# Kernel tuning notes

Hardware: AMD Instinct MI355X
Metric: run time of the kernel (lower is better)

The kernel has to match this reference:

```python
import jax, jax.numpy as jnp
import numpy as np

N = 50000        # nodes
E = 800000       # edges
H = 128          # in = hidden = out width
L = 4            # num_layers
BN_EPS = 1e-5


def _bn(x, g, b):
    # training-mode batch norm over the node dimension (biased variance, as torch)
    mu = jnp.mean(x, axis=0)
    var = jnp.mean((x - mu) ** 2, axis=0)
    return (x - mu) * jax.lax.rsqrt(var + BN_EPS) * g + b


def setup_inputs() -> dict:
    key = jax.random.key(0)
    ks = jax.random.split(key, 16)
    s = 0.05
    return {
        "x": jax.random.normal(ks[0], (N, H), dtype=jnp.float32),
        "edge_index": jax.random.randint(ks[1], (2, E), 0, N, dtype=jnp.int32),
        # stacked per-layer MLP params (all layers share dims H->H->H)
        "fc1_w": jax.random.normal(ks[2], (L, H, H), dtype=jnp.float32) * s,
        "fc1_b": jnp.zeros((L, H), dtype=jnp.float32),
        "bn1_g": jnp.ones((L, H), dtype=jnp.float32),
        "bn1_b": jnp.zeros((L, H), dtype=jnp.float32),
        "fc2_w": jax.random.normal(ks[3], (L, H, H), dtype=jnp.float32) * s,
        "fc2_b": jnp.zeros((L, H), dtype=jnp.float32),
        "bn2_g": jnp.ones((L, H), dtype=jnp.float32),
        "bn2_b": jnp.zeros((L, H), dtype=jnp.float32),
        # outer per-layer BatchNorm (intended one-per-GIN-layer)
        "bn3_g": jnp.ones((L, H), dtype=jnp.float32),
        "bn3_b": jnp.zeros((L, H), dtype=jnp.float32),
        # final classifier
        "fc_w": jax.random.normal(ks[4], (H, H), dtype=jnp.float32) * s,
        "fc_b": jnp.zeros((H,), dtype=jnp.float32),
    }


def reference(x, edge_index, fc1_w, fc1_b, bn1_g, bn1_b, fc2_w, fc2_b,
              bn2_g, bn2_b, bn3_g, bn3_b, fc_w, fc_b):
    src = edge_index[0]
    dst = edge_index[1]
    for i in range(L):
        # GINConv, eps=0: h = MLP((1+eps)*x + sum_{j in N(v)} x_j)
        agg = jax.ops.segment_sum(x[src], dst, num_segments=N)  # [N, H]
        h = x + agg
        # MLP: relu(bn1(fc1(h))) -> bn2(fc2(.))
        h = jax.nn.relu(_bn(h @ fc1_w[i].T + fc1_b[i], bn1_g[i], bn1_b[i]))
        h = _bn(h @ fc2_w[i].T + fc2_b[i], bn2_g[i], bn2_b[i])
        # outer BN + ReLU per layer
        x = jax.nn.relu(_bn(h, bn3_g[i], bn3_b[i]))
    return x @ fc_w.T + fc_b  # [N, H]
```

## Files before the change

kernel.cpp:

```cpp
#include <hip/hip_runtime.h>
#include <hip/hip_bf16.h>

#define NN 50000
#define HD 128
#define NL 4
#define BN_EPS 1e-5f
#define NTILES 3125

typedef __attribute__((ext_vector_type(8))) short short8;
typedef __attribute__((ext_vector_type(4))) float f32x4;

__device__ inline ushort f2bf(float f){
  uint u = __float_as_uint(f);
  uint r = (u + 0x7fffu + ((u >> 16) & 1u)) >> 16;
  return (ushort)r;
}
__device__ inline float bflo(uint u){ return __uint_as_float(u << 16); }
__device__ inline float bfhi(uint u){ return __uint_as_float(u & 0xffff0000u); }

__global__ void cast_f32_bf16x4(const float* __restrict__ in, ushort* __restrict__ out, int n4){
  int i = blockIdx.x * blockDim.x + threadIdx.x;
  int stride = gridDim.x * blockDim.x;
  const float4* in4 = (const float4*)in;
  for (; i < n4; i += stride){
    float4 v = in4[i];
    ushort4 r;
    r.x = f2bf(v.x); r.y = f2bf(v.y); r.z = f2bf(v.z); r.w = f2bf(v.w);
    *(ushort4*)(out + i * 4) = r;
  }
}

__global__ void cast_weights(const float* __restrict__ w1, const float* __restrict__ w2,
                             const float* __restrict__ wf, ushort* __restrict__ wb){
  int i = blockIdx.x * 256 + threadIdx.x;
  if (i >= 36864) return;
  const float* src;
  if (i < 16384)      src = w1 + i * 4;
  else if (i < 32768) src = w2 + (i - 16384) * 4;
  else                src = wf + (i - 32768) * 4;
  float4 v = *(const float4*)src;
  ushort4 r;
  r.x = f2bf(v.x); r.y = f2bf(v.y); r.z = f2bf(v.z); r.w = f2bf(v.w);
  *(ushort4*)(wb + i * 4) = r;
}

__global__ void fill1_kernel(const int* __restrict__ dst, int* __restrict__ cnt,
                             int* __restrict__ pos, int E){
  int e = (blockIdx.x * 256 + threadIdx.x) * 4;
  if (e + 4 <= E){
    int4 d = *(const int4*)(dst + e);
    int4 p;
    p.x = atomicAdd(&cnt[d.x], 1);
    p.y = atomicAdd(&cnt[d.y], 1);
    p.z = atomicAdd(&cnt[d.z], 1);
    p.w = atomicAdd(&cnt[d.w], 1);
    *(int4*)(pos + e) = p;
  } else {
    for (; e < E; ++e) pos[e] = atomicAdd(&cnt[dst[e]], 1);
  }
}

__global__ void scan1_kernel(const int* __restrict__ deg, int* __restrict__ incl,
                             int* __restrict__ bsum, int n){
  __shared__ int tmp[1024];
  int gid = blockIdx.x * 1024 + threadIdx.x;
  int v = (gid < n) ? deg[gid] : 0;
  tmp[threadIdx.x] = v;
  __syncthreads();
  for (int ofs = 1; ofs < 1024; ofs <<= 1){
    int t = tmp[threadIdx.x];
    int a = (threadIdx.x >= ofs) ? tmp[threadIdx.x - ofs] : 0;
    __syncthreads();
    tmp[threadIdx.x] = t + a;
    __syncthreads();
  }
  if (gid < n) incl[gid] = tmp[threadIdx.x];
  if (threadIdx.x == 1023) bsum[blockIdx.x] = tmp[1023];
}

__global__ void scan2_kernel(const int* __restrict__ bsum, int* __restrict__ base,
                             int* __restrict__ off, int nb, int n){
  if (threadIdx.x == 0){
    int run = 0;
    for (int i = 0; i < nb; ++i){ base[i] = run; run += bsum[i]; }
    off[n] = run;
  }
}

__global__ void scan3_kernel(const int* __restrict__ deg, const int* __restrict__ incl,
                             const int* __restrict__ base, int* __restrict__ off, int n){
  int gid = blockIdx.x * 1024 + threadIdx.x;
  if (gid < n) off[gid] = incl[gid] - deg[gid] + base[blockIdx.x];
}

__global__ void fill2_kernel(const int* __restrict__ src, const int* __restrict__ dst,
                             const int* __restrict__ off, const int* __restrict__ pos,
                             int* __restrict__ csrc, int E){
  int e = (blockIdx.x * 256 + threadIdx.x) * 4;
  if (e + 4 <= E){
    int4 d = *(const int4*)(dst + e);
    int4 p = *(const int4*)(pos + e);
    int4 s = *(const int4*)(src + e);
    csrc[off[d.x] + p.x] = s.x;
    csrc[off[d.y] + p.y] = s.y;
    csrc[off[d.z] + p.z] = s.z;
    csrc[off[d.w] + p.w] = s.w;
  } else {
    for (; e < E; ++e) csrc[off[dst[e]] + pos[e]] = src[e];
  }
}

__device__ inline void bn_params_tid(const float* st, const float* gA, const float* gB,
                                     const float* bB, int mode, float* sS, float* sT){
  int c = threadIdx.x;
  if (c < 128){
    const float invN = 1.f / (float)NN;
    float mu = st[c] * invN;
    float var = fmaxf(st[128 + c] * invN - mu * mu, 0.f);
    float S, T;
    if (mode == 0){
      S = gA[c] * rsqrtf(var + BN_EPS);
      T = gB[c] - mu * S;
    } else {
      float inv2 = rsqrtf(var + BN_EPS);
      float tt = gA[c] * inv2;
      float inv3 = rsqrtf(tt * tt * var + BN_EPS);
      S = tt * inv3 * gB[c];
      T = bB[c] - mu * S;
    }
    sS[c] = S; sT[c] = T;
  }
}

__global__ __launch_bounds__(256) void agg_kernel(const ushort* __restrict__ xb,
                                                  const int* __restrict__ off,
                                                  const int* __restrict__ csrc,
                                                  ushort* __restrict__ h){
  int node = blockIdx.x * 4 + (threadIdx.x >> 6);
  int lane = threadIdx.x & 63;
  const uint* xr = (const uint*)xb;
  uint self = xr[node * 64 + lane];
  float ax = bflo(self), ay = bfhi(self);
  int s = off[node], e = off[node + 1];
  int j = s;
  for (; j + 8 <= e; j += 8){
    uint v0 = xr[csrc[j+0]*64+lane], v1 = xr[csrc[j+1]*64+lane];
    uint v2 = xr[csrc[j+2]*64+lane], v3 = xr[csrc[j+3]*64+lane];
    uint v4 = xr[csrc[j+4]*64+lane], v5 = xr[csrc[j+5]*64+lane];
    uint v6 = xr[csrc[j+6]*64+lane], v7 = xr[csrc[j+7]*64+lane];
    ax += bflo(v0)+bflo(v1)+bflo(v2)+bflo(v3)+bflo(v4)+bflo(v5)+bflo(v6)+bflo(v7);
    ay += bfhi(v0)+bfhi(v1)+bfhi(v2)+bfhi(v3)+bfhi(v4)+bfhi(v5)+bfhi(v6)+bfhi(v7);
  }
  for (; j + 4 <= e; j += 4){
    uint v0 = xr[csrc[j+0]*64+lane], v1 = xr[csrc[j+1]*64+lane];
    uint v2 = xr[csrc[j+2]*64+lane], v3 = xr[csrc[j+3]*64+lane];
    ax += bflo(v0)+bflo(v1)+bflo(v2)+bflo(v3);
    ay += bfhi(v0)+bfhi(v1)+bfhi(v2)+bfhi(v3);
  }
  for (; j < e; ++j){
    uint v = xr[csrc[j] * 64 + lane];
    ax += bflo(v); ay += bfhi(v);
  }
  uint o = (uint)f2bf(ax) | ((uint)f2bf(ay) << 16);
  ((uint*)h)[node * 64 + lane] = o;
}

__global__ __launch_bounds__(256) void agg_bn_kernel(const ushort* __restrict__ yb,
                                                     const int* __restrict__ off,
                                                     const int* __restrict__ csrc,
                                                     const float* __restrict__ statsIn,
                                                     const float* __restrict__ g2,
                                                     const float* __restrict__ g3,
                                                     const float* __restrict__ b3,
                                                     ushort* __restrict__ h){
  __shared__ float sS[128];
  __shared__ float sT[128];
  bn_params_tid(statsIn, g2, g3, b3, 1, sS, sT);
  __syncthreads();
  int node = blockIdx.x * 4 + (threadIdx.x >> 6);
  int lane = threadIdx.x & 63;
  float S0 = sS[lane*2], T0 = sT[lane*2];
  float S1 = sS[lane*2+1], T1 = sT[lane*2+1];
  const uint* xr = (const uint*)yb;
  uint self = xr[node * 64 + lane];
  float ax = fmaxf(bflo(self)*S0+T0, 0.f), ay = fmaxf(bfhi(self)*S1+T1, 0.f);
  int s = off[node], e = off[node + 1];
  int j = s;
  for (; j + 4 <= e; j += 4){
    uint v0 = xr[csrc[j+0]*64+lane], v1 = xr[csrc[j+1]*64+lane];
    uint v2 = xr[csrc[j+2]*64+lane], v3 = xr[csrc[j+3]*64+lane];
    ax += fmaxf(bflo(v0)*S0+T0,0.f) + fmaxf(bflo(v1)*S0+T0,0.f)
        + fmaxf(bflo(v2)*S0+T0,0.f) + fmaxf(bflo(v3)*S0+T0,0.f);
    ay += fmaxf(bfhi(v0)*S1+T1,0.f) + fmaxf(bfhi(v1)*S1+T1,0.f)
        + fmaxf(bfhi(v2)*S1+T1,0.f) + fmaxf(bfhi(v3)*S1+T1,0.f);
  }
  for (; j < e; ++j){
    uint v = xr[csrc[j] * 64 + lane];
    ax += fmaxf(bflo(v)*S0+T0,0.f);
    ay += fmaxf(bfhi(v)*S1+T1,0.f);
  }
  uint o = (uint)f2bf(ax) | ((uint)f2bf(ay) << 16);
  ((uint*)h)[node * 64 + lane] = o;
}

__global__ __launch_bounds__(512) void gemm_kernel(const ushort* __restrict__ A,
                                                   const ushort* __restrict__ W,
                                                   const float* __restrict__ bias,
                                                   ushort* __restrict__ Yb,
                                                   float* __restrict__ Yf,
                                                   float* __restrict__ statsOut,
                                                   const float* __restrict__ statsIn,
                                                   const float* __restrict__ gA,
                                                   const float* __restrict__ gB,
                                                   const float* __restrict__ bB,
                                                   int mode){
  __shared__ uint4 w4[128 * 17];
  __shared__ float ssum[128];
  __shared__ float ssq[128];
  __shared__ float sS[128];
  __shared__ float sT[128];
  const uint4* Wg = (const uint4*)W;
  for (int c = threadIdx.x; c < 2048; c += 512){
    w4[(c >> 4) * 17 + (c & 15)] = Wg[c];
  }
  if (statsIn) bn_params_tid(statsIn, gA, gB, bB, mode, sS, sT);
  if (threadIdx.x < 128){ ssum[threadIdx.x] = 0.f; ssq[threadIdx.x] = 0.f; }
  __syncthreads();

  int wave = threadIdx.x >> 6;
  int lane = threadIdx.x & 63;
  int m = lane & 15, q = lane >> 4;
  int tile = blockIdx.x * 8 + wave;
  bool tv = tile < NTILES;
  const uint4* A4 = (const uint4*)A;

  f32x4 acc[8];
#pragma unroll
  for (int i = 0; i < 8; ++i) acc[i] = (f32x4)0.f;

#pragma unroll
  for (int kt = 0; kt < 4; ++kt){
    short8 af = (short8)0;
    if (tv){
      uint4 t = A4[(tile * 16 + m) * 16 + kt * 4 + q];
      if (statsIn){
        int kc = kt * 32 + q * 8;
        uint4 pk;
        pk.x = (uint)f2bf(fmaxf(bflo(t.x)*sS[kc+0]+sT[kc+0],0.f))
             | ((uint)f2bf(fmaxf(bfhi(t.x)*sS[kc+1]+sT[kc+1],0.f)) << 16);
        pk.y = (uint)f2bf(fmaxf(bflo(t.y)*sS[kc+2]+sT[kc+2],0.f))
             | ((uint)f2bf(fmaxf(bfhi(t.y)*sS[kc+3]+sT[kc+3],0.f)) << 16);
        pk.z = (uint)f2bf(fmaxf(bflo(t.z)*sS[kc+4]+sT[kc+4],0.f))
             | ((uint)f2bf(fmaxf(bfhi(t.z)*sS[kc+5]+sT[kc+5],0.f)) << 16);
        pk.w = (uint)f2bf(fmaxf(bflo(t.w)*sS[kc+6]+sT[kc+6],0.f))
             | ((uint)f2bf(fmaxf(bfhi(t.w)*sS[kc+7]+sT[kc+7],0.f)) << 16);
        t = pk;
      }
      af = *(short8*)&t;
    }
#pragma unroll
    for (int to = 0; to < 8; ++to){
      uint4 bw = w4[(to * 16 + m) * 17 + kt * 4 + q];
      acc[to] = __builtin_amdgcn_mfma_f32_16x16x32_bf16(af, *(short8*)&bw, acc[to], 0, 0, 0);
    }
  }

  bool dost = (statsOut != nullptr);
#pragma unroll
  for (int to = 0; to < 8; ++to){
    int col = to * 16 + m;
    float bc = bias[col];
    float ls = 0.f, lq = 0.f;
    if (tv){
#pragma unroll
      for (int r = 0; r < 4; ++r){
        float v = acc[to][r] + bc;
        int row = tile * 16 + q * 4 + r;
        if (Yb) Yb[row * 128 + col] = __builtin_bit_cast(ushort, f2bf(v));
        else    Yf[row * 128 + col] = v;
        ls += v; lq += v * v;
      }
    }
    if (dost){
      ls += __shfl_xor(ls, 16); lq += __shfl_xor(lq, 16);
      ls += __shfl_xor(ls, 32); lq += __shfl_xor(lq, 32);
      if (tv && q == 0){ atomicAdd(&ssum[col], ls); atomicAdd(&ssq[col], lq); }
    }
  }
  if (dost){
    __syncthreads();
    if (threadIdx.x < 128){
      atomicAdd(&statsOut[threadIdx.x], ssum[threadIdx.x]);
      atomicAdd(&statsOut[128 + threadIdx.x], ssq[threadIdx.x]);
    }
  }
}

extern "C" void kernel_launch(void* const* d_in, const int* in_sizes, int n_in,
                              void* d_out, int out_size, void* d_ws, size_t ws_size,
                              hipStream_t stream) {
  const float* x     = (const float*)d_in[0];
  const int*   ei    = (const int*)d_in[1];
  const float* fc1_w = (const float*)d_in[2];
  const float* fc1_b = (const float*)d_in[3];
  const float* bn1_g = (const float*)d_in[4];
  const float* bn1_b = (const float*)d_in[5];
  const float* fc2_w = (const float*)d_in[6];
  const float* fc2_b = (const float*)d_in[7];
  const float* bn2_g = (const float*)d_in[8];
  const float* bn3_g = (const float*)d_in[10];
  const float* bn3_b = (const float*)d_in[11];
  const float* fc_w  = (const float*)d_in[12];
  const float* fc_b  = (const float*)d_in[13];

  int E = in_sizes[1] / 2;
  const int* srcp = ei;
  const int* dstp = ei + E;

  char* ws = (char*)d_ws;
  int*    off    = (int*)(ws + 0);
  int*    cnt    = (int*)(ws + 200064);
  int*    pos    = (int*)(ws + 400128);
  int*    csrc   = (int*)(ws + 3600128);
  ushort* wb     = (ushort*)(ws + 6800128);
  float*  stats  = (float*)(ws + 7095040);
  int*    sscr   = (int*)(ws + 7103232);
  ushort* xb     = (ushort*)(ws + 7104256);
  ushort* hb     = (ushort*)(ws + 19904256);
  ushort* y1b    = (ushort*)(ws + 32704256);
  ushort* y2b    = (ushort*)(ws + 45504256);

  int* incl = csrc;
  int* bsum = sscr;
  int* base = sscr + 64;

  hipMemsetAsync(cnt, 0, 200064, stream);
  hipMemsetAsync(stats, 0, 8192, stream);

  cast_f32_bf16x4<<<2048, 256, 0, stream>>>(x, xb, NN * HD / 4);
  cast_weights<<<144, 256, 0, stream>>>(fc1_w, fc2_w, fc_w, wb);

  const int EB4 = (E / 4 + 255) / 256 + 1;
  const int SB = (NN + 1023) / 1024;
  fill1_kernel<<<EB4, 256, 0, stream>>>(dstp, cnt, pos, E);
  scan1_kernel<<<SB, 1024, 0, stream>>>(cnt, incl, bsum, NN);
  scan2_kernel<<<1, 64, 0, stream>>>(bsum, base, off, SB, NN);
  scan3_kernel<<<SB, 1024, 0, stream>>>(cnt, incl, base, off, NN);
  fill2_kernel<<<EB4, 256, 0, stream>>>(srcp, dstp, off, pos, csrc, E);

  const int gb = (NTILES + 7) / 8;

  for (int i = 0; i < NL; ++i){
    if (i == 0){
      agg_kernel<<<NN / 4, 256, 0, stream>>>(xb, off, csrc, hb);
    } else {
      agg_bn_kernel<<<NN / 4, 256, 0, stream>>>(y2b, off, csrc,
                                                stats + (i - 1) * 512 + 256,
                                                bn2_g + (i - 1) * 128,
                                                bn3_g + (i - 1) * 128,
                                                bn3_b + (i - 1) * 128, hb);
    }
    gemm_kernel<<<gb, 512, 0, stream>>>(hb, wb + i * 16384, fc1_b + i * 128,
                                        y1b, nullptr, stats + i * 512,
                                        nullptr, nullptr, nullptr, nullptr, 0);
    gemm_kernel<<<gb, 512, 0, stream>>>(y1b, wb + 65536 + i * 16384, fc2_b + i * 128,
                                        y2b, nullptr, stats + i * 512 + 256,
                                        stats + i * 512, bn1_g + i * 128,
                                        bn1_b + i * 128, nullptr, 0);
  }

  gemm_kernel<<<gb, 512, 0, stream>>>(y2b, wb + 131072, fc_b,
                                      nullptr, (float*)d_out, nullptr,
                                      stats + 3 * 512 + 256, bn2_g + 384,
                                      bn3_g + 384, bn3_b + 384, 1);
}
```

Before: 486.3 us.

## Derive BN1 stats from Gram matrix and fuse both MLP GEMMs per layer

BN1 mean and variance are now computed algebraically from the Gram matrix H^T H and the column sums of the aggregated features, plus the fc1 weights. This lets fc1, BN1, ReLU, fc2 and the BN2 stat accumulation run in one fused kernel with no y1 round trip through global memory. The CSR degree counters are also striped four ways per node to cut atomic contention in graph construction. The cost is extra Gram, reduce and param kernels per layer, and bias handling that assumes the fc1 bias cancels under batch norm.

```diff
diff --git a/kernel.cpp b/kernel.cpp
--- a/kernel.cpp
+++ b/kernel.cpp
@@ -6,6 +6,9 @@
 #define NL 4
 #define BN_EPS 1e-5f
 #define NTILES 3125
+#define N4 200000
+#define GBLK 256
+#define GROWS 196
 
 typedef __attribute__((ext_vector_type(8))) short short8;
 typedef __attribute__((ext_vector_type(4))) float f32x4;
@@ -44,19 +47,19 @@
   *(ushort4*)(wb + i * 4) = r;
 }
 
-__global__ void fill1_kernel(const int* __restrict__ dst, int* __restrict__ cnt,
+__global__ void fill1_kernel(const int* __restrict__ dst, int* __restrict__ cnt4,
                              int* __restrict__ pos, int E){
   int e = (blockIdx.x * 256 + threadIdx.x) * 4;
   if (e + 4 <= E){
     int4 d = *(const int4*)(dst + e);
     int4 p;
-    p.x = atomicAdd(&cnt[d.x], 1);
-    p.y = atomicAdd(&cnt[d.y], 1);
-    p.z = atomicAdd(&cnt[d.z], 1);
-    p.w = atomicAdd(&cnt[d.w], 1);
+    p.x = atomicAdd(&cnt4[d.x * 4 + 0], 1);
+    p.y = atomicAdd(&cnt4[d.y * 4 + 1], 1);
+    p.z = atomicAdd(&cnt4[d.z * 4 + 2], 1);
+    p.w = atomicAdd(&cnt4[d.w * 4 + 3], 1);
     *(int4*)(pos + e) = p;
   } else {
-    for (; e < E; ++e) pos[e] = atomicAdd(&cnt[dst[e]], 1);
+    for (; e < E; ++e) pos[e] = atomicAdd(&cnt4[dst[e] * 4 + (e & 3)], 1);
   }
 }
 
@@ -94,19 +97,19 @@
 }
 
 __global__ void fill2_kernel(const int* __restrict__ src, const int* __restrict__ dst,
-                             const int* __restrict__ off, const int* __restrict__ pos,
+                             const int* __restrict__ off4, const int* __restrict__ pos,
                              int* __restrict__ csrc, int E){
   int e = (blockIdx.x * 256 + threadIdx.x) * 4;
   if (e + 4 <= E){
     int4 d = *(const int4*)(dst + e);
     int4 p = *(const int4*)(pos + e);
     int4 s = *(const int4*)(src + e);
-    csrc[off[d.x] + p.x] = s.x;
-    csrc[off[d.y] + p.y] = s.y;
-    csrc[off[d.z] + p.z] = s.z;
-    csrc[off[d.w] + p.w] = s.w;
+    csrc[off4[d.x * 4 + 0] + p.x] = s.x;
+    csrc[off4[d.y * 4 + 1] + p.y] = s.y;
+    csrc[off4[d.z * 4 + 2] + p.z] = s.z;
+    csrc[off4[d.w * 4 + 3] + p.w] = s.w;
   } else {
-    for (; e < E; ++e) csrc[off[dst[e]] + pos[e]] = src[e];
+    for (; e < E; ++e) csrc[off4[dst[e] * 4 + (e & 3)] + pos[e]] = src[e];
   }
 }
 
@@ -133,7 +136,7 @@
 }
 
 __global__ __launch_bounds__(256) void agg_kernel(const ushort* __restrict__ xb,
-                                                  const int* __restrict__ off,
+                                                  const int* __restrict__ off4,
                                                   const int* __restrict__ csrc,
                                                   ushort* __restrict__ h){
   int node = blockIdx.x * 4 + (threadIdx.x >> 6);
@@ -141,7 +144,7 @@
   const uint* xr = (const uint*)xb;
   uint self = xr[node * 64 + lane];
   float ax = bflo(self), ay = bfhi(self);
-  int s = off[node], e = off[node + 1];
+  int s = off4[node * 4], e = off4[node * 4 + 4];
   int j = s;
   for (; j + 8 <= e; j += 8){
     uint v0 = xr[csrc[j+0]*64+lane], v1 = xr[csrc[j+1]*64+lane];
@@ -166,7 +169,7 @@
 }
 
 __global__ __launch_bounds__(256) void agg_bn_kernel(const ushort* __restrict__ yb,
-                                                     const int* __restrict__ off,
+                                                     const int* __restrict__ off4,
                                                      const int* __restrict__ csrc,
                                                      const float* __restrict__ statsIn,
                                                      const float* __restrict__ g2,
@@ -184,7 +187,7 @@
   const uint* xr = (const uint*)yb;
   uint self = xr[node * 64 + lane];
   float ax = fmaxf(bflo(self)*S0+T0, 0.f), ay = fmaxf(bfhi(self)*S1+T1, 0.f);
-  int s = off[node], e = off[node + 1];
+  int s = off4[node * 4], e = off4[node * 4 + 4];
   int j = s;
   for (; j + 4 <= e; j += 4){
     uint v0 = xr[csrc[j+0]*64+lane], v1 = xr[csrc[j+1]*64+lane];
@@ -203,28 +206,266 @@
   ((uint*)h)[node * 64 + lane] = o;
 }
 
-__global__ __launch_bounds__(512) void gemm_kernel(const ushort* __restrict__ A,
-                                                   const ushort* __restrict__ W,
-                                                   const float* __restrict__ bias,
-                                                   ushort* __restrict__ Yb,
-                                                   float* __restrict__ Yf,
-                                                   float* __restrict__ statsOut,
-                                                   const float* __restrict__ statsIn,
-                                                   const float* __restrict__ gA,
-                                                   const float* __restrict__ gB,
-                                                   const float* __restrict__ bB,
-                                                   int mode){
+__global__ __launch_bounds__(256) void gram_kernel(const ushort* __restrict__ A,
+                                                   float* __restrict__ Gpart,
+                                                   float* __restrict__ spart){
+  __shared__ ushort at[128 * 40];
+  __shared__ float scl[512];
+  int t = threadIdx.x;
+  int wave = t >> 6, lane = t & 63;
+  int m = lane & 15, q = lane >> 4;
+  int cp = t & 63;
+  int rsub = t >> 6;
+  int rbase = blockIdx.x * GROWS;
+  const uint* A32 = (const uint*)A;
+  float sx = 0.f, sy = 0.f;
+  f32x4 acc[2][8];
+#pragma unroll
+  for (int i = 0; i < 2; ++i)
+#pragma unroll
+    for (int j = 0; j < 8; ++j) acc[i][j] = (f32x4)0.f;
+
+  for (int c0 = 0; c0 < GROWS; c0 += 32){
+#pragma unroll
+    for (int i = 0; i < 8; ++i){
+      int rr = rsub * 8 + i;
+      int r = rbase + c0 + rr;
+      uint u = 0;
+      if (r < NN && (c0 + rr) < GROWS) u = A32[r * 64 + cp];
+      at[(2 * cp) * 40 + rr] = (ushort)(u & 0xffffu);
+      at[(2 * cp + 1) * 40 + rr] = (ushort)(u >> 16);
+      sx += bflo(u); sy += bfhi(u);
+    }
+    __syncthreads();
+    short8 afr[2];
+#pragma unroll
+    for (int I = 0; I < 2; ++I){
+      uint4 ta = *(const uint4*)&at[((2 * wave + I) * 16 + m) * 40 + q * 8];
+      afr[I] = *(short8*)&ta;
+    }
+#pragma unroll
+    for (int J = 0; J < 8; ++J){
+      uint4 tb = *(const uint4*)&at[(J * 16 + m) * 40 + q * 8];
+      short8 bfr = *(short8*)&tb;
+      acc[0][J] = __builtin_amdgcn_mfma_f32_16x16x32_bf16(afr[0], bfr, acc[0][J], 0,0,0);
+      acc[1][J] = __builtin_amdgcn_mfma_f32_16x16x32_bf16(afr[1], bfr, acc[1][J], 0,0,0);
+    }
+    __syncthreads();
+  }
+
+  float* gp = Gpart + blockIdx.x * 16384;
+#pragma unroll
+  for (int I = 0; I < 2; ++I){
+#pragma unroll
+    for (int J = 0; J < 8; ++J){
+#pragma unroll
+      for (int r = 0; r < 4; ++r){
+        int row = (2 * wave + I) * 16 + q * 4 + r;
+        int col = J * 16 + m;
+        gp[row * 128 + col] = acc[I][J][r];
+      }
+    }
+  }
+  scl[(rsub * 64 + cp) * 2 + 0] = sx;
+  scl[(rsub * 64 + cp) * 2 + 1] = sy;
+  __syncthreads();
+  if (t < 64){
+    float ax = scl[t*2] + scl[(64+t)*2] + scl[(128+t)*2] + scl[(192+t)*2];
+    float ay = scl[t*2+1] + scl[(64+t)*2+1] + scl[(128+t)*2+1] + scl[(192+t)*2+1];
+    spart[blockIdx.x * 128 + 2*t] = ax;
+    spart[blockIdx.x * 128 + 2*t + 1] = ay;
+  }
+}
+
+__global__ void gram_reduce(const float* __restrict__ Gpart, const float* __restrict__ spart,
+                            float* __restrict__ G, float* __restrict__ svec){
+  int id = blockIdx.x * 256 + threadIdx.x;
+  if (id < 16384){
+    float a = 0.f;
+    for (int p = 0; p < GBLK; ++p) a += Gpart[p * 16384 + id];
+    G[id] = a;
+  } else if (id < 16512){
+    int c = id - 16384;
+    float a = 0.f;
+    for (int p = 0; p < GBLK; ++p) a += spart[p * 128 + c];
+    svec[c] = a;
+  }
+}
+
+__global__ __launch_bounds__(256) void param1_kernel(const float* __restrict__ G,
+                                                     const float* __restrict__ svec,
+                                                     const ushort* __restrict__ W1b,
+                                                     const float* __restrict__ g1,
+                                                     const float* __restrict__ bb1,
+                                                     float* __restrict__ params1){
+  __shared__ float wf[128];
+  __shared__ float red[256];
+  int c = blockIdx.x, t = threadIdx.x;
+  const uint* w32 = (const uint*)W1b + c * 64;
+  if (t < 64){ uint u = w32[t]; wf[2*t] = bflo(u); wf[2*t+1] = bfhi(u); }
+  __syncthreads();
+  float acc = 0.f;
+  for (int idx = t; idx < 16384; idx += 256)
+    acc += G[idx] * wf[idx >> 7] * wf[idx & 127];
+  red[t] = acc;
+  __syncthreads();
+  for (int o = 128; o > 0; o >>= 1){ if (t < o) red[t] += red[t + o]; __syncthreads(); }
+  float qq = red[0];
+  __syncthreads();
+  red[t] = (t < 128) ? wf[t] * svec[t] : 0.f;
+  __syncthreads();
+  for (int o = 128; o > 0; o >>= 1){ if (t < o) red[t] += red[t + o]; __syncthreads(); }
+  if (t == 0){
+    const float invN = 1.f / (float)NN;
+    float meanZ = red[0] * invN;
+    float var = fmaxf(qq * invN - meanZ * meanZ, 0.f);
+    float S = g1[c] * rsqrtf(var + BN_EPS);
+    params1[c] = S;
+    params1[128 + c] = bb1[c] - meanZ * S;
+  }
+}
+
+__global__ __launch_bounds__(512) void fused_mlp(const ushort* __restrict__ hb,
+                                                 const ushort* __restrict__ w1g,
+                                                 const ushort* __restrict__ w2g,
+                                                 const float* __restrict__ b2v,
+                                                 const float* __restrict__ params1,
+                                                 float* __restrict__ statsOut,
+                                                 ushort* __restrict__ y2b){
+  extern __shared__ char dyn[];
+  uint4* w1 = (uint4*)dyn;
+  uint4* w2 = (uint4*)(dyn + 34816);
+  float* sS = (float*)(dyn + 69632);
+  float* sT = sS + 128;
+  float* ssum = sT + 128;
+  float* ssq = ssum + 128;
+  int t = threadIdx.x, wave = t >> 6, lane = t & 63;
+  int m = lane & 15, q = lane >> 4;
+  int tile = blockIdx.x * 8 + wave;
+  bool tv = tile < NTILES;
+  const uint4* W1g = (const uint4*)w1g;
+  const uint4* W2g = (const uint4*)w2g;
+  for (int c = t; c < 2048; c += 512){
+    int d = (c >> 4) * 17 + (c & 15);
+    w1[d] = W1g[c];
+    w2[d] = W2g[c];
+  }
+  if (t < 128){
+    sS[t] = params1[t]; sT[t] = params1[128 + t];
+    ssum[t] = 0.f; ssq[t] = 0.f;
+  }
+  __syncthreads();
+
+  short8 af[4];
+  if (tv){
+    const uint4* A4 = (const uint4*)hb;
+#pragma unroll
+    for (int kt = 0; kt < 4; ++kt){
+      uint4 tt = A4[(tile * 16 + m) * 16 + kt * 4 + q];
+      af[kt] = *(short8*)&tt;
+    }
+  }
+
+  f32x4 acc[8];
+#pragma unroll
+  for (int i = 0; i < 8; ++i) acc[i] = (f32x4)0.f;
+  if (tv){
+#pragma unroll
+    for (int kt = 0; kt < 4; ++kt){
+#pragma unroll
+      for (int to = 0; to < 8; ++to){
+        uint4 bw = w1[(to*16+m)*17 + kt*4 + q];
+        acc[to] = __builtin_amdgcn_mfma_f32_16x16x32_bf16(af[kt], *(short8*)&bw, acc[to], 0,0,0);
+      }
+    }
+  }
+  __syncthreads();
+
+  uint* myscr = ((uint*)w1) + wave * 1088;
+  if (tv){
+#pragma unroll
+    for (int to = 0; to < 8; ++to){
+      int col = to * 16 + m;
+      float S = sS[col], T = sT[col];
+#pragma unroll
+      for (int r = 0; r < 4; ++r){
+        float v = fmaxf(acc[to][r] * S + T, 0.f);
+        uint u = f2bf(v);
+        uint other = (uint)__shfl_xor((int)u, 1);
+        if (!(m & 1)) myscr[(q*4+r)*68 + to*8 + (m>>1)] = u | (other << 16);
+      }
+    }
+#pragma unroll
+    for (int kt = 0; kt < 4; ++kt){
+      uint4 tt = *(const uint4*)(myscr + m * 68 + kt * 16 + q * 4);
+      af[kt] = *(short8*)&tt;
+    }
+  }
+
+#pragma unroll
+  for (int i = 0; i < 8; ++i) acc[i] = (f32x4)0.f;
+  if (tv){
+#pragma unroll
+    for (int kt = 0; kt < 4; ++kt){
+#pragma unroll
+      for (int to = 0; to < 8; ++to){
+        uint4 bw = w2[(to*16+m)*17 + kt*4 + q];
+        acc[to] = __builtin_amdgcn_mfma_f32_16x16x32_bf16(af[kt], *(short8*)&bw, acc[to], 0,0,0);
+      }
+    }
+#pragma unroll
+    for (int to = 0; to < 8; ++to){
+      float bc = b2v[to*16+m];
+#pragma unroll
+      for (int r = 0; r < 4; ++r) acc[to][r] += bc;
+    }
+  }
+
+#pragma unroll
+  for (int to = 0; to < 8; ++to){
+    float ls = 0.f, lq = 0.f;
+    if (tv){
+#pragma unroll
+      for (int r = 0; r < 4; ++r){ float v = acc[to][r]; ls += v; lq += v*v; }
+    }
+    ls += __shfl_xor(ls, 16); lq += __shfl_xor(lq, 16);
+    ls += __shfl_xor(ls, 32); lq += __shfl_xor(lq, 32);
+    if (tv && q == 0){ atomicAdd(&ssum[to*16+m], ls); atomicAdd(&ssq[to*16+m], lq); }
+  }
+  __syncthreads();
+  if (t < 128){
+    atomicAdd(&statsOut[t], ssum[t]);
+    atomicAdd(&statsOut[128 + t], ssq[t]);
+  }
+  if (tv){
+#pragma unroll
+    for (int to = 0; to < 8; ++to){
+      int col = to * 16 + m;
+#pragma unroll
+      for (int r = 0; r < 4; ++r){
+        int row = tile * 16 + q * 4 + r;
+        y2b[row * 128 + col] = __builtin_bit_cast(ushort, f2bf(acc[to][r]));
+      }
+    }
+  }
+}
+
+__global__ __launch_bounds__(512) void gemm_cls(const ushort* __restrict__ A,
+                                                const ushort* __restrict__ W,
+                                                const float* __restrict__ bias,
+                                                float* __restrict__ Yf,
+                                                const float* __restrict__ statsIn,
+                                                const float* __restrict__ gA,
+                                                const float* __restrict__ gB,
+                                                const float* __restrict__ bB){
   __shared__ uint4 w4[128 * 17];
-  __shared__ float ssum[128];
-  __shared__ float ssq[128];
   __shared__ float sS[128];
   __shared__ float sT[128];
   const uint4* Wg = (const uint4*)W;
   for (int c = threadIdx.x; c < 2048; c += 512){
     w4[(c >> 4) * 17 + (c & 15)] = Wg[c];
   }
-  if (statsIn) bn_params_tid(statsIn, gA, gB, bB, mode, sS, sT);
-  if (threadIdx.x < 128){ ssum[threadIdx.x] = 0.f; ssq[threadIdx.x] = 0.f; }
+  bn_params_tid(statsIn, gA, gB, bB, 1, sS, sT);
   __syncthreads();
 
   int wave = threadIdx.x >> 6;
@@ -242,21 +483,18 @@
   for (int kt = 0; kt < 4; ++kt){
     short8 af = (short8)0;
     if (tv){
-      uint4 t = A4[(tile * 16 + m) * 16 + kt * 4 + q];
-      if (statsIn){
-        int kc = kt * 32 + q * 8;
-        uint4 pk;
-        pk.x = (uint)f2bf(fmaxf(bflo(t.x)*sS[kc+0]+sT[kc+0],0.f))
-             | ((uint)f2bf(fmaxf(bfhi(t.x)*sS[kc+1]+sT[kc+1],0.f)) << 16);
-        pk.y = (uint)f2bf(fmaxf(bflo(t.y)*sS[kc+2]+sT[kc+2],0.f))
-             | ((uint)f2bf(fmaxf(bfhi(t.y)*sS[kc+3]+sT[kc+3],0.f)) << 16);
-        pk.z = (uint)f2bf(fmaxf(bflo(t.z)*sS[kc+4]+sT[kc+4],0.f))
-             | ((uint)f2bf(fmaxf(bfhi(t.z)*sS[kc+5]+sT[kc+5],0.f)) << 16);
-        pk.w = (uint)f2bf(fmaxf(bflo(t.w)*sS[kc+6]+sT[kc+6],0.f))
-             | ((uint)f2bf(fmaxf(bfhi(t.w)*sS[kc+7]+sT[kc+7],0.f)) << 16);
-        t = pk;
-      }
-      af = *(short8*)&t;
+      uint4 tt = A4[(tile * 16 + m) * 16 + kt * 4 + q];
+      int kc = kt * 32 + q * 8;
+      uint4 pk;
+      pk.x = (uint)f2bf(fmaxf(bflo(tt.x)*sS[kc+0]+sT[kc+0],0.f))
+           | ((uint)f2bf(fmaxf(bfhi(tt.x)*sS[kc+1]+sT[kc+1],0.f)) << 16);
+      pk.y = (uint)f2bf(fmaxf(bflo(tt.y)*sS[kc+2]+sT[kc+2],0.f))
+           | ((uint)f2bf(fmaxf(bfhi(tt.y)*sS[kc+3]+sT[kc+3],0.f)) << 16);
+      pk.z = (uint)f2bf(fmaxf(bflo(tt.z)*sS[kc+4]+sT[kc+4],0.f))
+           | ((uint)f2bf(fmaxf(bfhi(tt.z)*sS[kc+5]+sT[kc+5],0.f)) << 16);
+      pk.w = (uint)f2bf(fmaxf(bflo(tt.w)*sS[kc+6]+sT[kc+6],0.f))
+           | ((uint)f2bf(fmaxf(bfhi(tt.w)*sS[kc+7]+sT[kc+7],0.f)) << 16);
+      af = *(short8*)&pk;
     }
 #pragma unroll
     for (int to = 0; to < 8; ++to){
@@ -265,33 +503,14 @@
     }
   }
 
-  bool dost = (statsOut != nullptr);
-#pragma unroll
-  for (int to = 0; to < 8; ++to){
-    int col = to * 16 + m;
-    float bc = bias[col];
-    float ls = 0.f, lq = 0.f;
-    if (tv){
-#pragma unroll
-      for (int r = 0; r < 4; ++r){
-        float v = acc[to][r] + bc;
-        int row = tile * 16 + q * 4 + r;
-        if (Yb) Yb[row * 128 + col] = __builtin_bit_cast(ushort, f2bf(v));
-        else    Yf[row * 128 + col] = v;
-        ls += v; lq += v * v;
-      }
-    }
-    if (dost){
-      ls += __shfl_xor(ls, 16); lq += __shfl_xor(lq, 16);
-      ls += __shfl_xor(ls, 32); lq += __shfl_xor(lq, 32);
-      if (tv && q == 0){ atomicAdd(&ssum[col], ls); atomicAdd(&ssq[col], lq); }
-    }
-  }
-  if (dost){
-    __syncthreads();
-    if (threadIdx.x < 128){
-      atomicAdd(&statsOut[threadIdx.x], ssum[threadIdx.x]);
-      atomicAdd(&statsOut[128 + threadIdx.x], ssq[threadIdx.x]);
+  if (tv){
+#pragma unroll
+    for (int to = 0; to < 8; ++to){
+      int col = to * 16 + m;
+      float bc = bias[col];
+#pragma unroll
+      for (int r = 0; r < 4; ++r)
+        Yf[(tile * 16 + q * 4 + r) * 128 + col] = acc[to][r] + bc;
     }
   }
 }
@@ -312,65 +531,72 @@
   const float* bn3_b = (const float*)d_in[11];
   const float* fc_w  = (const float*)d_in[12];
   const float* fc_b  = (const float*)d_in[13];
+  (void)fc1_b;
 
   int E = in_sizes[1] / 2;
   const int* srcp = ei;
   const int* dstp = ei + E;
 
   char* ws = (char*)d_ws;
-  int*    off    = (int*)(ws + 0);
-  int*    cnt    = (int*)(ws + 200064);
-  int*    pos    = (int*)(ws + 400128);
-  int*    csrc   = (int*)(ws + 3600128);
-  ushort* wb     = (ushort*)(ws + 6800128);
-  float*  stats  = (float*)(ws + 7095040);
-  int*    sscr   = (int*)(ws + 7103232);
-  ushort* xb     = (ushort*)(ws + 7104256);
-  ushort* hb     = (ushort*)(ws + 19904256);
-  ushort* y1b    = (ushort*)(ws + 32704256);
-  ushort* y2b    = (ushort*)(ws + 45504256);
+  int*    off4    = (int*)(ws + 0);
+  int*    cnt4    = (int*)(ws + 3200064);
+  int*    pos     = (int*)(ws + 6400064);
+  int*    csrc    = (int*)(ws + 9600064);
+  ushort* wb      = (ushort*)(ws + 12800064);
+  float*  stats   = (float*)(ws + 13094976);
+  int*    sscr    = (int*)(ws + 13099072);
+  float*  params1 = (float*)(ws + 13103168);
+  float*  G       = (float*)(ws + 13104192);
+  float*  svec    = (float*)(ws + 13169728);
+  float*  Gpart   = (float*)(ws + 13170240);
+  float*  spart   = (float*)(ws + 29947456);
+  ushort* xb      = (ushort*)(ws + 30078528);
+  ushort* hb      = (ushort*)(ws + 42878528);
+  ushort* y2b     = (ushort*)(ws + 55678528);
 
   int* incl = csrc;
   int* bsum = sscr;
-  int* base = sscr + 64;
-
-  hipMemsetAsync(cnt, 0, 200064, stream);
-  hipMemsetAsync(stats, 0, 8192, stream);
+  int* base = sscr + 512;
+
+  hipMemsetAsync(cnt4, 0, 3200000, stream);
+  hipMemsetAsync(stats, 0, 4096, stream);
 
   cast_f32_bf16x4<<<2048, 256, 0, stream>>>(x, xb, NN * HD / 4);
   cast_weights<<<144, 256, 0, stream>>>(fc1_w, fc2_w, fc_w, wb);
 
   const int EB4 = (E / 4 + 255) / 256 + 1;
-  const int SB = (NN + 1023) / 1024;
-  fill1_kernel<<<EB4, 256, 0, stream>>>(dstp, cnt, pos, E);
-  scan1_kernel<<<SB, 1024, 0, stream>>>(cnt, incl, bsum, NN);
-  scan2_kernel<<<1, 64, 0, stream>>>(bsum, base, off, SB, NN);
-  scan3_kernel<<<SB, 1024, 0, stream>>>(cnt, incl, base, off, NN);
-  fill2_kernel<<<EB4, 256, 0, stream>>>(srcp, dstp, off, pos, csrc, E);
+  const int SB4 = (N4 + 1023) / 1024;
+  fill1_kernel<<<EB4, 256, 0, stream>>>(dstp, cnt4, pos, E);
+  scan1_kernel<<<SB4, 1024, 0, stream>>>(cnt4, incl, bsum, N4);
+  scan2_kernel<<<1, 64, 0, stream>>>(bsum, base, off4, SB4, N4);
+  scan3_kernel<<<SB4, 1024, 0, stream>>>(cnt4, incl, base, off4, N4);
+  fill2_kernel<<<EB4, 256, 0, stream>>>(srcp, dstp, off4, pos, csrc, E);
+
+  hipFuncSetAttribute((const void*)fused_mlp,
+                      hipFuncAttributeMaxDynamicSharedMemorySize, 71680);
 
   const int gb = (NTILES + 7) / 8;
 
-  for (int i = 0; i < NL; ++i){
-    if (i == 0){
-      agg_kernel<<<NN / 4, 256, 0, stream>>>(xb, off, csrc, hb);
+  for (int L = 0; L < NL; ++L){
+    if (L == 0){
+      agg_kernel<<<NN / 4, 256, 0, stream>>>(xb, off4, csrc, hb);
     } else {
-      agg_bn_kernel<<<NN / 4, 256, 0, stream>>>(y2b, off, csrc,
-                                                stats + (i - 1) * 512 + 256,
-                                                bn2_g + (i - 1) * 128,
-                                                bn3_g + (i - 1) * 128,
-                                                bn3_b + (i - 1) * 128, hb);
-    }
-    gemm_kernel<<<gb, 512, 0, stream>>>(hb, wb + i * 16384, fc1_b + i * 128,
-                                        y1b, nullptr, stats + i * 512,
-                                        nullptr, nullptr, nullptr, nullptr, 0);
-    gemm_kernel<<<gb, 512, 0, stream>>>(y1b, wb + 65536 + i * 16384, fc2_b + i * 128,
-                                        y2b, nullptr, stats + i * 512 + 256,
-                                        stats + i * 512, bn1_g + i * 128,
-                                        bn1_b + i * 128, nullptr, 0);
-  }
-
-  gemm_kernel<<<gb, 512, 0, stream>>>(y2b, wb + 131072, fc_b,
-                                      nullptr, (float*)d_out, nullptr,
-                                      stats + 3 * 512 + 256, bn2_g + 384,
-                                      bn3_g + 384, bn3_b + 384, 1);
-}
+      agg_bn_kernel<<<NN / 4, 256, 0, stream>>>(y2b, off4, csrc,
+                                                stats + (L - 1) * 256,
+                                                bn2_g + (L - 1) * 128,
+                                                bn3_g + (L - 1) * 128,
+                                                bn3_b + (L - 1) * 128, hb);
+    }
+    gram_kernel<<<GBLK, 256, 0, stream>>>(hb, Gpart, spart);
+    gram_reduce<<<65, 256, 0, stream>>>(Gpart, spart, G, svec);
+    param1_kernel<<<128, 256, 0, stream>>>(G, svec, wb + L * 16384,
+                                           bn1_g + L * 128, bn1_b + L * 128, params1);
+    fused_mlp<<<gb, 512, 71680, stream>>>(hb, wb + L * 16384, wb + 65536 + L * 16384,
+                                          fc2_b + L * 128, params1,
+                                          stats + L * 256, y2b);
+  }
+
+  gemm_cls<<<gb, 512, 0, stream>>>(y2b, wb + 131072, fc_b, (float*)d_out,
+                                   stats + 3 * 256, bn2_g + 384,
+                                   bn3_g + 384, bn3_b + 384);
+}
```

New measurement: 634.0 us. 1.3x slower.
